# Kernel tuning notes

Hardware: AMD Instinct MI355X
Metric: run time of the kernel (lower is better)

The kernel has to match this reference:

```python
import jax, jax.numpy as jnp
import numpy as np

P = 64          # num_populations
T = 8192        # buffer_size (buffer assumed full / all valid)
K = 8           # num_bins
HIST = 2        # history_length
NPAST = K ** HIST          # number of single-series past states
NCOMB = NPAST * NPAST      # joint (y_past, x_past) states
N = T - HIST - 1           # n_samples per pair


def _discretize(x):
    # Faithful to torch _discretize: min-max normalize, floor into K bins.
    xmin = x.min()
    xmax = x.max()
    rng = xmax - xmin
    norm = (x - xmin) / (rng + 1e-8)
    b = jnp.clip((norm * (K - 1)).astype(jnp.int32), 0, K - 1)
    return jnp.where(rng < 1e-8, jnp.zeros_like(b), b)


def _cond_entropy(counts, state_mask):
    # counts: (S, K) histogram of y_future per conditioning state.
    # Torch skips states with total count < 2; weight = count/N.
    tot = counts.sum(axis=1)                          # (S,)
    valid = (tot >= 2.0) & state_mask
    p = counts / jnp.maximum(tot[:, None], 1.0)
    p_safe = jnp.where(counts > 0, p, 1.0)
    h = -jnp.where(counts > 0, p * jnp.log2(p_safe), 0.0).sum(axis=1)
    w = tot / N
    return jnp.where(valid, w * h, 0.0).sum()


def _te(src_d, tgt_d):
    # src_d, tgt_d: (T,) int bins. TE(src -> tgt) in bits.
    yf = tgt_d[HIST + 1: HIST + 1 + N]                # y_future, (N,)
    # hash of k-step histories: sum_i K**i * series[k-i : k-i+N]
    yp = sum((K ** i) * tgt_d[HIST - i: HIST - i + N] for i in range(HIST))
    xp = sum((K ** i) * src_d[HIST - i: HIST - i + N] for i in range(HIST))
    # joint histograms via scatter-add (the fused histogram kernel target)
    cy = jnp.zeros((NPAST, K), jnp.float32).at[yp, yf].add(1.0)
    cc = jnp.zeros((NCOMB, K), jnp.float32).at[yp * NPAST + xp, yf].add(1.0)
    # torch loops yp in range(min(NPAST, N)) -> mask out higher state ids
    mask_y = jnp.arange(NPAST) < min(NPAST, N)
    h_y_given_yp = _cond_entropy(cy, mask_y)
    h_y_given_ypxp = _cond_entropy(cc, jnp.ones((NCOMB,), dtype=bool))
    return jnp.maximum(0.0, h_y_given_yp - h_y_given_ypxp)


def setup_inputs() -> dict:
    key = jax.random.key(0)
    return {"time_series": jax.random.normal(key, (T, P), dtype=jnp.float32)}


def reference(time_series):
    # time_series: (T, P). Returns flow_matrix (P, P): flow[i, j] = TE(i -> j).
    d = jax.vmap(_discretize, in_axes=1, out_axes=0)(time_series)  # (P, T) int
    flow = jax.vmap(lambda s: jax.vmap(lambda t: _te(s, t))(d))(d)  # (P, P)
    return flow * (1.0 - jnp.eye(P, dtype=flow.dtype))  # diagonal forced to 0
```

## Files before the change

### kernel.cpp

```cpp
#include <hip/hip_runtime.h>

static constexpr int T = 8192;
static constexpr int P = 64;
static constexpr int NSAMP = 8189;

__global__ __launch_bounds__(256) void prep_kernel(const float* __restrict__ ts,
        unsigned short* __restrict__ A, unsigned short* __restrict__ X,
        float* __restrict__ h_y)
{
    __shared__ float col[T];
    __shared__ unsigned char bins[T];
    __shared__ unsigned int cy[512];
    __shared__ float wred[16];
    const int p = blockIdx.x, tid = threadIdx.x;
    const int lane = tid & 63, wave = tid >> 6;

    float mn = 3.402823466e38f, mx = -3.402823466e38f;
    for (int t = tid; t < T; t += 256) {
        float v = ts[t * P + p];
        col[t] = v;
        mn = fminf(mn, v);
        mx = fmaxf(mx, v);
    }
    #pragma unroll
    for (int off = 32; off > 0; off >>= 1) {
        mn = fminf(mn, __shfl_down(mn, off, 64));
        mx = fmaxf(mx, __shfl_down(mx, off, 64));
    }
    if (lane == 0) { wred[wave] = mn; wred[4 + wave] = mx; }
    for (int i = tid; i < 512; i += 256) cy[i] = 0u;
    __syncthreads();
    const float xmin = fminf(fminf(wred[0], wred[1]), fminf(wred[2], wred[3]));
    const float xmax = fmaxf(fmaxf(wred[4], wred[5]), fmaxf(wred[6], wred[7]));
    const float rng = xmax - xmin;
    const float den = rng + 1e-8f;
    const int flat = rng < 1e-8f;

    for (int t = tid; t < T; t += 256) {
        float norm = (col[t] - xmin) / den;
        int b = (int)(norm * 7.0f);
        b = b < 0 ? 0 : (b > 7 ? 7 : b);
        bins[t] = flat ? (unsigned char)0 : (unsigned char)b;
    }
    __syncthreads();

    unsigned short* Ap = A + p * T;
    unsigned short* Xp = X + p * T;
    for (int i = tid * 4; i + 3 < NSAMP; i += 1024) {
        unsigned w0 = *(const unsigned*)&bins[i];
        unsigned w1 = *(const unsigned*)&bins[i + 4];
        unsigned long long bb = (unsigned long long)w0 | ((unsigned long long)w1 << 32);
        ushort4 av, xv;
        unsigned short* ap = (unsigned short*)&av;
        unsigned short* xp = (unsigned short*)&xv;
        #pragma unroll
        for (int j = 0; j < 4; ++j) {
            unsigned b1 = (unsigned)(bb >> (8 * (j + 1))) & 255u;
            unsigned b2 = (unsigned)(bb >> (8 * (j + 2))) & 255u;
            unsigned b3 = (unsigned)(bb >> (8 * (j + 3))) & 255u;
            unsigned yp = b2 + 8u * b1;
            ap[j] = (unsigned short)(yp * 512u + b3);
            xp[j] = (unsigned short)(yp * 8u);
            atomicAdd(&cy[yp * 8u + b3], 1u);
        }
        *(ushort4*)(Ap + i) = av;
        *(ushort4*)(Xp + i) = xv;
    }
    if (tid == 0) {
        unsigned b1 = bins[NSAMP], b2 = bins[NSAMP + 1], b3 = bins[NSAMP + 2];
        unsigned yp = b2 + 8u * b1;
        Ap[NSAMP - 1] = (unsigned short)(yp * 512u + b3);
        Xp[NSAMP - 1] = (unsigned short)(yp * 8u);
        atomicAdd(&cy[yp * 8u + b3], 1u);
    }
    __syncthreads();

    if (tid < 64) {
        float tot = 0.0f, sc = 0.0f;
        #pragma unroll
        for (int v = 0; v < 8; ++v) {
            unsigned c = cy[tid * 8 + v];
            if (c) { float fc = (float)c; tot += fc; sc += fc * log2f(fc); }
        }
        float acc = (tot >= 2.0f) ? (tot * log2f(tot) - sc) : 0.0f;
        #pragma unroll
        for (int off = 32; off > 0; off >>= 1) acc += __shfl_down(acc, off, 64);
        if (tid == 0) h_y[p] = acc * (1.0f / (float)NSAMP);
    }
}

__global__ __launch_bounds__(256) void pair_kernel(const unsigned short* __restrict__ A,
        const unsigned short* __restrict__ X, const float* __restrict__ h_y,
        float* __restrict__ out)
{
    const int src = blockIdx.x >> 6, tgt = blockIdx.x & 63, tid = threadIdx.x;
    if (src == tgt) { if (tid == 0) out[blockIdx.x] = 0.0f; return; }

    __shared__ unsigned int hj[8192];
    __shared__ float lut[256];
    __shared__ float red[4];

    for (int c = tid; c < 256; c += 256) {
        float fc = (float)c;
        float f0 = (c == 0) ? 0.0f : fc * log2f(fc);
        lut[c] = (fc + 1.0f) * log2f(fc + 1.0f) - f0;
    }
    uint4* z = (uint4*)hj;
    for (int i = tid; i < 2048; i += 256) z[i] = make_uint4(0u, 0u, 0u, 0u);
    __syncthreads();

    const unsigned short* At = A + tgt * T;
    const unsigned short* Xs = X + src * T;
    float acc = 0.0f;

    auto step = [&](unsigned a, unsigned x) {
        unsigned jc = a + x;
        unsigned st = jc >> 3, yf = jc & 7u;
        unsigned scr = (st * 0x2C5u) & 4095u;
        unsigned cell = (scr << 3) | yf;
        unsigned w = cell >> 2, sh = (cell & 3u) << 3;
        unsigned oldv = atomicAdd(&hj[w], 1u << sh);
        unsigned oc = (oldv >> sh) & 255u;
        acc -= lut[oc];
    };

    for (int i = tid * 4; i + 3 < NSAMP; i += 1024) {
        ushort4 a4 = *(const ushort4*)(At + i);
        ushort4 x4 = *(const ushort4*)(Xs + i);
        step(a4.x, x4.x); step(a4.y, x4.y); step(a4.z, x4.z); step(a4.w, x4.w);
    }
    if (tid == 0) step(At[NSAMP - 1], Xs[NSAMP - 1]);
    __syncthreads();

    for (int st = tid; st < 4096; st += 256) {
        unsigned base = ((st * 0x2C5u) & 4095u) * 2u;
        uint2 wv = *(const uint2*)&hj[base];
        unsigned s0 = (wv.x & 0x00FF00FFu) + ((wv.x >> 8) & 0x00FF00FFu);
        unsigned s1 = (wv.y & 0x00FF00FFu) + ((wv.y >> 8) & 0x00FF00FFu);
        unsigned s = s0 + s1;
        unsigned tot = (s & 0xFFFFu) + (s >> 16);
        if (tot) { float ft = (float)tot; acc += ft * log2f(ft); }
    }

    #pragma unroll
    for (int off = 32; off > 0; off >>= 1) acc += __shfl_down(acc, off, 64);
    if ((tid & 63) == 0) red[tid >> 6] = acc;
    __syncthreads();
    if (tid == 0) {
        float h2 = (red[0] + red[1] + red[2] + red[3]) * (1.0f / (float)NSAMP);
        out[blockIdx.x] = fmaxf(0.0f, h_y[tgt] - h2);
    }
}

extern "C" void kernel_launch(void* const* d_in, const int* in_sizes, int n_in,
                              void* d_out, int out_size, void* d_ws, size_t ws_size,
                              hipStream_t stream)
{
    const float* ts = (const float*)d_in[0];
    float* out = (float*)d_out;
    unsigned short* A = (unsigned short*)d_ws;
    unsigned short* X = A + P * T;
    float* h_y = (float*)(X + P * T);

    prep_kernel<<<dim3(P), dim3(256), 0, stream>>>(ts, A, X, h_y);
    pair_kernel<<<dim3(P * P), dim3(256), 0, stream>>>(A, X, h_y, out);
}
```

Before: 103.1 us.

## Compute joint entropy from final histogram instead of incremental LUT updates

```diff
diff --git a/kernel.cpp b/kernel.cpp
--- a/kernel.cpp
+++ b/kernel.cpp
@@ -4,19 +4,19 @@
 static constexpr int P = 64;
 static constexpr int NSAMP = 8189;
 
-__global__ __launch_bounds__(256) void prep_kernel(const float* __restrict__ ts,
+__global__ __launch_bounds__(1024) void prep_kernel(const float* __restrict__ ts,
         unsigned short* __restrict__ A, unsigned short* __restrict__ X,
         float* __restrict__ h_y)
 {
     __shared__ float col[T];
     __shared__ unsigned char bins[T];
     __shared__ unsigned int cy[512];
-    __shared__ float wred[16];
+    __shared__ float wred[32];
     const int p = blockIdx.x, tid = threadIdx.x;
     const int lane = tid & 63, wave = tid >> 6;
 
     float mn = 3.402823466e38f, mx = -3.402823466e38f;
-    for (int t = tid; t < T; t += 256) {
+    for (int t = tid; t < T; t += 1024) {
         float v = ts[t * P + p];
         col[t] = v;
         mn = fminf(mn, v);
@@ -27,16 +27,20 @@
         mn = fminf(mn, __shfl_down(mn, off, 64));
         mx = fmaxf(mx, __shfl_down(mx, off, 64));
     }
-    if (lane == 0) { wred[wave] = mn; wred[4 + wave] = mx; }
-    for (int i = tid; i < 512; i += 256) cy[i] = 0u;
+    if (lane == 0) { wred[wave] = mn; wred[16 + wave] = mx; }
+    for (int i = tid; i < 512; i += 1024) cy[i] = 0u;
     __syncthreads();
-    const float xmin = fminf(fminf(wred[0], wred[1]), fminf(wred[2], wred[3]));
-    const float xmax = fmaxf(fmaxf(wred[4], wred[5]), fmaxf(wred[6], wred[7]));
+    float xmin = wred[0], xmax = wred[16];
+    #pragma unroll
+    for (int j = 1; j < 16; ++j) {
+        xmin = fminf(xmin, wred[j]);
+        xmax = fmaxf(xmax, wred[16 + j]);
+    }
     const float rng = xmax - xmin;
     const float den = rng + 1e-8f;
     const int flat = rng < 1e-8f;
 
-    for (int t = tid; t < T; t += 256) {
+    for (int t = tid; t < T; t += 1024) {
         float norm = (col[t] - xmin) / den;
         int b = (int)(norm * 7.0f);
         b = b < 0 ? 0 : (b > 7 ? 7 : b);
@@ -46,7 +50,7 @@
 
     unsigned short* Ap = A + p * T;
     unsigned short* Xp = X + p * T;
-    for (int i = tid * 4; i + 3 < NSAMP; i += 1024) {
+    for (int i = tid * 4; i + 3 < NSAMP; i += 4096) {
         unsigned w0 = *(const unsigned*)&bins[i];
         unsigned w1 = *(const unsigned*)&bins[i + 4];
         unsigned long long bb = (unsigned long long)w0 | ((unsigned long long)w1 << 32);
@@ -97,49 +101,54 @@
     if (src == tgt) { if (tid == 0) out[blockIdx.x] = 0.0f; return; }
 
     __shared__ unsigned int hj[8192];
-    __shared__ float lut[256];
     __shared__ float red[4];
 
-    for (int c = tid; c < 256; c += 256) {
-        float fc = (float)c;
-        float f0 = (c == 0) ? 0.0f : fc * log2f(fc);
-        lut[c] = (fc + 1.0f) * log2f(fc + 1.0f) - f0;
-    }
     uint4* z = (uint4*)hj;
     for (int i = tid; i < 2048; i += 256) z[i] = make_uint4(0u, 0u, 0u, 0u);
     __syncthreads();
 
     const unsigned short* At = A + tgt * T;
     const unsigned short* Xs = X + src * T;
-    float acc = 0.0f;
 
     auto step = [&](unsigned a, unsigned x) {
         unsigned jc = a + x;
         unsigned st = jc >> 3, yf = jc & 7u;
         unsigned scr = (st * 0x2C5u) & 4095u;
         unsigned cell = (scr << 3) | yf;
-        unsigned w = cell >> 2, sh = (cell & 3u) << 3;
-        unsigned oldv = atomicAdd(&hj[w], 1u << sh);
-        unsigned oc = (oldv >> sh) & 255u;
-        acc -= lut[oc];
+        atomicAdd(&hj[cell >> 2], 1u << ((cell & 3u) << 3));
     };
 
-    for (int i = tid * 4; i + 3 < NSAMP; i += 1024) {
-        ushort4 a4 = *(const ushort4*)(At + i);
-        ushort4 x4 = *(const ushort4*)(Xs + i);
-        step(a4.x, x4.x); step(a4.y, x4.y); step(a4.z, x4.z); step(a4.w, x4.w);
+    for (int i = tid * 8; i + 7 < NSAMP; i += 2048) {
+        uint4 aw = *(const uint4*)(At + i);
+        uint4 xw = *(const uint4*)(Xs + i);
+        step(aw.x & 0xffffu, xw.x & 0xffffu); step(aw.x >> 16, xw.x >> 16);
+        step(aw.y & 0xffffu, xw.y & 0xffffu); step(aw.y >> 16, xw.y >> 16);
+        step(aw.z & 0xffffu, xw.z & 0xffffu); step(aw.z >> 16, xw.z >> 16);
+        step(aw.w & 0xffffu, xw.w & 0xffffu); step(aw.w >> 16, xw.w >> 16);
     }
-    if (tid == 0) step(At[NSAMP - 1], Xs[NSAMP - 1]);
+    if (tid < 5) step(At[8184 + tid], Xs[8184 + tid]);
     __syncthreads();
 
-    for (int st = tid; st < 4096; st += 256) {
-        unsigned base = ((st * 0x2C5u) & 4095u) * 2u;
-        uint2 wv = *(const uint2*)&hj[base];
-        unsigned s0 = (wv.x & 0x00FF00FFu) + ((wv.x >> 8) & 0x00FF00FFu);
-        unsigned s1 = (wv.y & 0x00FF00FFu) + ((wv.y >> 8) & 0x00FF00FFu);
-        unsigned s = s0 + s1;
-        unsigned tot = (s & 0xFFFFu) + (s >> 16);
-        if (tot) { float ft = (float)tot; acc += ft * log2f(ft); }
+    float acc = 0.0f;
+    for (int s = tid; s < 4096; s += 256) {
+        uint2 wv = *(const uint2*)&hj[s * 2];
+        unsigned w0 = wv.x, w1 = wv.y;
+        unsigned s01 = (w0 & 0x00FF00FFu) + ((w0 >> 8) & 0x00FF00FFu);
+        unsigned s23 = (w1 & 0x00FF00FFu) + ((w1 >> 8) & 0x00FF00FFu);
+        unsigned ss = s01 + s23;
+        unsigned tot = (ss & 0xFFFFu) + (ss >> 16);
+        if (tot >= 2u) {
+            float sc = 0.0f;
+            #pragma unroll
+            for (int b = 0; b < 4; ++b) {
+                float f0 = (float)((w0 >> (8 * b)) & 255u);
+                float f1 = (float)((w1 >> (8 * b)) & 255u);
+                sc += f0 * __log2f(fmaxf(f0, 1.0f));
+                sc += f1 * __log2f(fmaxf(f1, 1.0f));
+            }
+            float ft = (float)tot;
+            acc += ft * __log2f(ft) - sc;
+        }
     }
 
     #pragma unroll
@@ -162,6 +171,6 @@
     unsigned short* X = A + P * T;
     float* h_y = (float*)(X + P * T);
 
-    prep_kernel<<<dim3(P), dim3(256), 0, stream>>>(ts, A, X, h_y);
+    prep_kernel<<<dim3(P), dim3(1024), 0, stream>>>(ts, A, X, h_y);
     pair_kernel<<<dim3(P * P), dim3(256), 0, stream>>>(A, X, h_y, out);
 }
```

Result: no change. 104.1 us (+1.0%).
